# Optimization experiments

Hardware: AMD Instinct MI355X
Metric: run time of the kernel (lower is better)

Reference implementation:

```python
import jax, jax.numpy as jnp
import numpy as np

N, NODE_DIM, EDGE_DIM, HID, NREL = 1024, 128, 32, 128, 16


def _sage(h, adj, W, b):
    # agg = mean over (weighted) neighbors: (adj @ h) / (deg + 1e-6)
    agg = (adj @ h) / (jnp.sum(adj, axis=1, keepdims=True) + 1e-6)
    return jax.nn.relu(jnp.concatenate([h, agg], axis=1) @ W.T + b)


def setup_inputs() -> dict:
    key = jax.random.key(0)
    ks = jax.random.split(key, 12)
    s1 = 1.0 / np.sqrt(2 * NODE_DIM)
    s2 = 1.0 / np.sqrt(2 * HID)
    s3 = 1.0 / np.sqrt(2 * HID + EDGE_DIM)
    s4 = 1.0 / np.sqrt(HID)
    return {
        "node_feat": jax.random.normal(ks[0], (N, NODE_DIM), jnp.float32),
        "edge_feat": jax.random.normal(ks[1], (N, N, EDGE_DIM), jnp.float32),
        "adj": jax.random.uniform(ks[2], (N, N), jnp.float32),
        "W_g1": jax.random.normal(ks[3], (HID, 2 * NODE_DIM), jnp.float32) * s1,
        "b_g1": jax.random.normal(ks[4], (HID,), jnp.float32) * s1,
        "W_g2": jax.random.normal(ks[5], (HID, 2 * HID), jnp.float32) * s2,
        "b_g2": jax.random.normal(ks[6], (HID,), jnp.float32) * s2,
        "W_c1": jax.random.normal(ks[7], (HID, 2 * HID + EDGE_DIM), jnp.float32) * s3,
        "b_c1": jax.random.normal(ks[8], (HID,), jnp.float32) * s3,
        "W_c2": jax.random.normal(ks[9], (NREL, HID), jnp.float32) * s4,
        "b_c2": jax.random.normal(ks[10], (NREL,), jnp.float32) * s4,
    }


def reference(node_feat, edge_feat, adj, W_g1, b_g1, W_g2, b_g2, W_c1, b_c1, W_c2, b_c2):
    h = _sage(node_feat, adj, W_g1, b_g1)          # [N, HID]
    h = _sage(h, adj, W_g2, b_g2)                  # [N, HID]
    H = h.shape[1]
    # Split first classifier layer over [h_i ; h_j ; e_ij] to avoid a huge concat.
    Wa, Wb, We = W_c1[:, :H], W_c1[:, H:2 * H], W_c1[:, 2 * H:]
    pre = ((h @ Wa.T)[:, None, :]
           + (h @ Wb.T)[None, :, :]
           + jnp.einsum('ije,he->ijh', edge_feat, We)
           + b_c1)                                  # [N, N, HID]
    logits = jax.nn.relu(pre) @ W_c2.T + b_c2       # [N, N, NREL]
    # diagonal (i == j) stays zero, matching the skipped loop iterations
    n = logits.shape[0]
    mask = 1.0 - jnp.eye(n, dtype=logits.dtype)
    return logits * mask[:, :, None]
```

## Files before the change

### kernel.cpp

```cpp
#include <hip/hip_runtime.h>
#include <hip/hip_bf16.h>
#include <stdint.h>

constexpr int NN = 1024;
constexpr int DD = 128;
constexpr int EDIM = 32;
constexpr int NR = 16;

using short4v = __attribute__((ext_vector_type(4))) short;
using short8v = __attribute__((ext_vector_type(8))) short;
using f32x4   = __attribute__((ext_vector_type(4))) float;

__device__ __forceinline__ short f2bf(float x) {
  __hip_bfloat16 h = __float2bfloat16(x);
  return __builtin_bit_cast(short, h);
}

__device__ __forceinline__ void nt_store4(float* p, const float4& v) {
  f32x4 t;
  t[0] = v.x; t[1] = v.y; t[2] = v.z; t[3] = v.w;
  __builtin_nontemporal_store(t, (f32x4*)p);
}

__global__ __launch_bounds__(256) void k_adjmm(const float* __restrict__ X,
                                               const float* __restrict__ adj,
                                               float* __restrict__ part) {
  __shared__ short xt[32][264];
  int t = threadIdx.x;
  int w = t >> 6, lane = t & 63;
  int c = lane & 15, g = lane >> 4;
  int b = blockIdx.x;
  int ic = b & 15, hc = (b >> 4) & 3, kc = b >> 6;
  int i0 = ic * 64 + w * 16, h0 = hc * 32;
  int k0 = kc * 256;

  {
    const float* xr = X + (size_t)(k0 + t) * DD + h0;
    #pragma unroll
    for (int c8 = 0; c8 < 4; ++c8) {
      float4 v0 = *(const float4*)(xr + c8 * 8);
      float4 v1 = *(const float4*)(xr + c8 * 8 + 4);
      xt[c8 * 8 + 0][t] = f2bf(v0.x);
      xt[c8 * 8 + 1][t] = f2bf(v0.y);
      xt[c8 * 8 + 2][t] = f2bf(v0.z);
      xt[c8 * 8 + 3][t] = f2bf(v0.w);
      xt[c8 * 8 + 4][t] = f2bf(v1.x);
      xt[c8 * 8 + 5][t] = f2bf(v1.y);
      xt[c8 * 8 + 6][t] = f2bf(v1.z);
      xt[c8 * 8 + 7][t] = f2bf(v1.w);
    }
  }
  __syncthreads();

  f32x4 acc0 = {0, 0, 0, 0}, acc1 = {0, 0, 0, 0};
  const short* xa0 = &xt[c][8 * g];
  const short* xa1 = &xt[16 + c][8 * g];
  const float* ba  = adj + (size_t)(i0 + c) * NN + k0 + 8 * g;
  #pragma unroll
  for (int ks = 0; ks < 8; ++ks) {
    short8v a0 = *(const short8v*)(xa0 + ks * 32);
    short8v a1 = *(const short8v*)(xa1 + ks * 32);
    float4 b0 = *(const float4*)(ba + ks * 32);
    float4 b1 = *(const float4*)(ba + ks * 32 + 4);
    short8v bb;
    bb[0] = f2bf(b0.x); bb[1] = f2bf(b0.y); bb[2] = f2bf(b0.z); bb[3] = f2bf(b0.w);
    bb[4] = f2bf(b1.x); bb[5] = f2bf(b1.y); bb[6] = f2bf(b1.z); bb[7] = f2bf(b1.w);
    acc0 = __builtin_amdgcn_mfma_f32_16x16x32_bf16(a0, bb, acc0, 0, 0, 0);
    acc1 = __builtin_amdgcn_mfma_f32_16x16x32_bf16(a1, bb, acc1, 0, 0, 0);
  }
  float* p0 = part + ((size_t)kc * NN + (i0 + c)) * DD + h0 + 4 * g;
  float4 o0 = {acc0[0], acc0[1], acc0[2], acc0[3]};
  float4 o1 = {acc1[0], acc1[1], acc1[2], acc1[3]};
  *(float4*)(p0)      = o0;
  *(float4*)(p0 + 16) = o1;
}

__global__ __launch_bounds__(256) void k_dense1(const float* __restrict__ X,
                                                const float* __restrict__ part,
                                                const float* __restrict__ adj,
                                                const float* __restrict__ W,
                                                const float* __restrict__ b,
                                                float* __restrict__ out,
                                                float* __restrict__ rsinv) {
  __shared__ float sagg[2][128];
  __shared__ float red[4];
  int t = threadIdx.x;
  int ig = t >> 7, h = t & 127;
  int i = blockIdx.x * 2 + ig;
  {
    const float4* ar = (const float4*)(adj + (size_t)i * NN);
    float4 v0 = ar[h * 2], v1 = ar[h * 2 + 1];
    float s = v0.x + v0.y + v0.z + v0.w + v1.x + v1.y + v1.z + v1.w;
    #pragma unroll
    for (int off = 32; off > 0; off >>= 1) s += __shfl_down(s, off, 64);
    if ((t & 63) == 0) red[t >> 6] = s;
  }
  __syncthreads();
  float rs = 1.0f / (red[ig * 2] + red[ig * 2 + 1] + 1e-6f);
  if (h == 0) rsinv[i] = rs;
  {
    float ss = 0.f;
    #pragma unroll
    for (int kc = 0; kc < 4; ++kc) ss += part[(size_t)kc * NN * DD + (size_t)i * DD + h];
    sagg[ig][h] = ss * rs;
  }
  __syncthreads();
  const float4* xr = (const float4*)(X + (size_t)i * DD);
  const float4* ar = (const float4*)(&sagg[ig][0]);
  const float4* w1 = (const float4*)(W + (size_t)h * 256);
  const float4* w2 = (const float4*)(W + (size_t)h * 256 + DD);
  float acc = b[h];
  #pragma unroll 8
  for (int k = 0; k < 32; ++k) {
    float4 x = xr[k], w = w1[k];
    acc += x.x * w.x + x.y * w.y + x.z * w.z + x.w * w.w;
  }
  #pragma unroll 8
  for (int k = 0; k < 32; ++k) {
    float4 y = ar[k], w = w2[k];
    acc += y.x * w.x + y.y * w.y + y.z * w.z + y.w * w.w;
  }
  out[(size_t)i * DD + h] = fmaxf(acc, 0.f);
}

__global__ __launch_bounds__(256) void k_dense2ab(const float* __restrict__ X,
                                                  const float* __restrict__ part,
                                                  const float* __restrict__ rsinv,
                                                  const float* __restrict__ W,
                                                  const float* __restrict__ b,
                                                  const float* __restrict__ Wc1,
                                                  const float* __restrict__ bc1,
                                                  float* __restrict__ Aib,
                                                  float* __restrict__ Bmat) {
  __shared__ float sagg[2][128];
  __shared__ float sh2[2][128];
  int t = threadIdx.x;
  int ig = t >> 7, h = t & 127;
  int i = blockIdx.x * 2 + ig;
  {
    float ss = 0.f;
    #pragma unroll
    for (int kc = 0; kc < 4; ++kc) ss += part[(size_t)kc * NN * DD + (size_t)i * DD + h];
    sagg[ig][h] = ss * rsinv[i];
  }
  __syncthreads();
  {
    const float4* xr = (const float4*)(X + (size_t)i * DD);
    const float4* ar = (const float4*)(&sagg[ig][0]);
    const float4* w1 = (const float4*)(W + (size_t)h * 256);
    const float4* w2 = (const float4*)(W + (size_t)h * 256 + DD);
    float acc = b[h];
    #pragma unroll 8
    for (int k = 0; k < 32; ++k) {
      float4 x = xr[k], w = w1[k];
      acc += x.x * w.x + x.y * w.y + x.z * w.z + x.w * w.w;
    }
    #pragma unroll 8
    for (int k = 0; k < 32; ++k) {
      float4 y = ar[k], w = w2[k];
      acc += y.x * w.x + y.y * w.y + y.z * w.z + y.w * w.w;
    }
    sh2[ig][h] = fmaxf(acc, 0.f);
  }
  __syncthreads();
  const float4* xr = (const float4*)(&sh2[ig][0]);
  const float4* wa = (const float4*)(Wc1 + (size_t)h * 288);
  const float4* wb = (const float4*)(Wc1 + (size_t)h * 288 + 128);
  float aa = bc1[h], bb = 0.f;
  #pragma unroll 8
  for (int k = 0; k < 32; ++k) {
    float4 x = xr[k];
    float4 a = wa[k], b2 = wb[k];
    aa += x.x * a.x + x.y * a.y + x.z * a.z + x.w * a.w;
    bb += x.x * b2.x + x.y * b2.y + x.z * b2.z + x.w * b2.w;
  }
  Aib[(size_t)i * DD + h] = aa;
  Bmat[(size_t)i * DD + h] = bb;
}

#define EDGE_BODY(T, S, PF) do {                                              \
    float4 a_ = eA##S, b_ = eB##S;                                            \
    if (PF) {                                                                 \
      const float* p_ = ebl + (size_t)((T) + 6) * ((size_t)NN * EDIM);        \
      eA##S = *(const float4*)p_;                                             \
      eB##S = *(const float4*)(p_ + 4);                                       \
    }                                                                         \
    short8v ef_;                                                              \
    ef_[0]=f2bf(a_.x); ef_[1]=f2bf(a_.y); ef_[2]=f2bf(a_.z); ef_[3]=f2bf(a_.w); \
    ef_[4]=f2bf(b_.x); ef_[5]=f2bf(b_.y); ef_[6]=f2bf(b_.z); ef_[7]=f2bf(b_.w); \
    char* pw_ = psm + (((T) & 1) << 12);                                      \
    const float* ap_ = aibs + (T) * 128 + 4 * g;                              \
    _Pragma("unroll")                                                         \
    for (int n = 0; n < 8; ++n) {                                             \
      float4 av_ = *(const float4*)(ap_ + 16 * n);                            \
      f32x4 ci_;                                                              \
      ci_[0] = av_.x + bjv[n].x; ci_[1] = av_.y + bjv[n].y;                   \
      ci_[2] = av_.z + bjv[n].z; ci_[3] = av_.w + bjv[n].w;                   \
      f32x4 acc_ = __builtin_amdgcn_mfma_f32_16x16x32_bf16(weF[n], ef_, ci_, 0, 0, 0); \
      short4v pk_;                                                            \
      pk_[0] = f2bf(fmaxf(acc_[0], 0.f)); pk_[1] = f2bf(fmaxf(acc_[1], 0.f)); \
      pk_[2] = f2bf(fmaxf(acc_[2], 0.f)); pk_[3] = f2bf(fmaxf(acc_[3], 0.f)); \
      *(short4v*)(pw_ + (((n >> 1) << 10) + ((n & 1) << 9) + wroff)) = pk_;   \
    }                                                                         \
  } while (0)

#define G2(G2T, OREG) do {                                                    \
    f32x4 a2_;                                                                \
    a2_[0] = bc2v.x; a2_[1] = bc2v.y; a2_[2] = bc2v.z; a2_[3] = bc2v.w;       \
    const char* pp_ = psm + (((G2T) & 1) << 12);                              \
    _Pragma("unroll")                                                         \
    for (int kk = 0; kk < 4; ++kk) {                                          \
      short8v pb_ = *(const short8v*)(pp_ + ((kk << 10) + rdP));              \
      a2_ = __builtin_amdgcn_mfma_f32_16x16x32_bf16(wcF[kk], pb_, a2_, 0, 0, 0); \
    }                                                                         \
    bool dg_ = (j == i0 + (G2T));                                             \
    OREG.x = dg_ ? 0.f : a2_[0];                                              \
    OREG.y = dg_ ? 0.f : a2_[1];                                              \
    OREG.z = dg_ ? 0.f : a2_[2];                                              \
    OREG.w = dg_ ? 0.f : a2_[3];                                              \
  } while (0)

#define FLUSH(BASE) do {                                                      \
    nt_store4(out + ((size_t)(i0 + (BASE) + 0) * NN + j) * NR + 4 * g, o0);   \
    nt_store4(out + ((size_t)(i0 + (BASE) + 1) * NN + j) * NR + 4 * g, o1);   \
    nt_store4(out + ((size_t)(i0 + (BASE) + 2) * NN + j) * NR + 4 * g, o2);   \
    nt_store4(out + ((size_t)(i0 + (BASE) + 3) * NN + j) * NR + 4 * g, o3);   \
  } while (0)

__global__ __launch_bounds__(256, 1) void k_edge(const float* __restrict__ edge,
                                                 const float* __restrict__ Wc1,
                                                 const float* __restrict__ Wc2,
                                                 const float* __restrict__ bc2,
                                                 const float* __restrict__ Aib,
                                                 const float* __restrict__ Bmat,
                                                 float* __restrict__ out) {
  __shared__ __align__(16) char psm_all[4][2][4096];
  __shared__ __align__(16) float aibs[16 * 128];
  int tid = threadIdx.x;
  int w = tid >> 6, lane = tid & 63;
  int c = lane & 15, g = lane >> 4;
  int ig = blockIdx.x >> 4, jg = blockIdx.x & 15;
  int i0 = ig * 16;
  int j0w = jg * 64 + w * 16;
  int j = j0w + c;

  {
    int ii = tid >> 4, h8 = (tid & 15) * 8;
    const float4* s = (const float4*)(Aib + (size_t)(i0 + ii) * DD + h8);
    *(float4*)(aibs + ii * 128 + h8)     = s[0];
    *(float4*)(aibs + ii * 128 + h8 + 4) = s[1];
  }

  short8v weF[8];
  #pragma unroll
  for (int n = 0; n < 8; ++n) {
    const float* p = Wc1 + (size_t)(16 * n + c) * 288 + 256 + 8 * g;
    float4 f0 = *(const float4*)p;
    float4 f1 = *(const float4*)(p + 4);
    short8v s;
    s[0]=f2bf(f0.x); s[1]=f2bf(f0.y); s[2]=f2bf(f0.z); s[3]=f2bf(f0.w);
    s[4]=f2bf(f1.x); s[5]=f2bf(f1.y); s[6]=f2bf(f1.z); s[7]=f2bf(f1.w);
    weF[n] = s;
  }
  short8v wcF[4];
  #pragma unroll
  for (int kk = 0; kk < 4; ++kk) {
    const float* p = Wc2 + (size_t)c * DD + 32 * kk + 8 * g;
    float4 f0 = *(const float4*)p;
    float4 f1 = *(const float4*)(p + 4);
    short8v s;
    s[0]=f2bf(f0.x); s[1]=f2bf(f0.y); s[2]=f2bf(f0.z); s[3]=f2bf(f0.w);
    s[4]=f2bf(f1.x); s[5]=f2bf(f1.y); s[6]=f2bf(f1.z); s[7]=f2bf(f1.w);
    wcF[kk] = s;
  }
  float4 bc2v = *(const float4*)(bc2 + 4 * g);
  float4 bjv[8];
  #pragma unroll
  for (int n = 0; n < 8; ++n)
    bjv[n] = *(const float4*)(Bmat + (size_t)j * DD + 16 * n + 4 * g);

  __syncthreads();

  char* psm = &psm_all[w][0][0];
  const float* ebl = edge + ((size_t)i0 * NN + j) * EDIM + 8 * g;
  int wroff = (c << 4) + ((g & 1) << 3) + ((g >> 1) << 8);
  int rdP   = (g << 8) + (c << 4);

  float4 o0, o1, o2, o3;

  float4 eA0, eB0, eA1, eB1, eA2, eB2, eA3, eB3, eA4, eB4, eA5, eB5;
  {
    const size_t STP = (size_t)NN * EDIM;
    eA0 = *(const float4*)(ebl);            eB0 = *(const float4*)(ebl + 4);
    eA1 = *(const float4*)(ebl + STP);      eB1 = *(const float4*)(ebl + STP + 4);
    eA2 = *(const float4*)(ebl + 2 * STP);  eB2 = *(const float4*)(ebl + 2 * STP + 4);
    eA3 = *(const float4*)(ebl + 3 * STP);  eB3 = *(const float4*)(ebl + 3 * STP + 4);
    eA4 = *(const float4*)(ebl + 4 * STP);  eB4 = *(const float4*)(ebl + 4 * STP + 4);
    eA5 = *(const float4*)(ebl + 5 * STP);  eB5 = *(const float4*)(ebl + 5 * STP + 4);
  }

  EDGE_BODY(0, 0, 1);
  EDGE_BODY(1, 1, 1);  G2(0, o0);
  EDGE_BODY(2, 2, 1);  G2(1, o1);
  EDGE_BODY(3, 3, 1);  G2(2, o2);
  EDGE_BODY(4, 4, 1);  G2(3, o3);  FLUSH(0);
  EDGE_BODY(5, 5, 1);  G2(4, o0);
  EDGE_BODY(6, 0, 1);  G2(5, o1);
  EDGE_BODY(7, 1, 1);  G2(6, o2);
  EDGE_BODY(8, 2, 1);  G2(7, o3);  FLUSH(4);
  EDGE_BODY(9, 3, 1);  G2(8, o0);
  EDGE_BODY(10, 4, 0); G2(9, o1);
  EDGE_BODY(11, 5, 0); G2(10, o2);
  EDGE_BODY(12, 0, 0); G2(11, o3); FLUSH(8);
  EDGE_BODY(13, 1, 0); G2(12, o0);
  EDGE_BODY(14, 2, 0); G2(13, o1);
  EDGE_BODY(15, 3, 0); G2(14, o2);
  G2(15, o3); FLUSH(12);
}

extern "C" void kernel_launch(void* const* d_in, const int* in_sizes, int n_in,
                              void* d_out, int out_size, void* d_ws, size_t ws_size,
                              hipStream_t stream) {
  const float* node_feat = (const float*)d_in[0];
  const float* edge_feat = (const float*)d_in[1];
  const float* adj  = (const float*)d_in[2];
  const float* W_g1 = (const float*)d_in[3];
  const float* b_g1 = (const float*)d_in[4];
  const float* W_g2 = (const float*)d_in[5];
  const float* b_g2 = (const float*)d_in[6];
  const float* W_c1 = (const float*)d_in[7];
  const float* b_c1 = (const float*)d_in[8];
  const float* W_c2 = (const float*)d_in[9];
  const float* b_c2 = (const float*)d_in[10];
  float* out = (float*)d_out;

  float* ws    = (float*)d_ws;
  float* rsinv = ws;
  float* part  = ws + 1024;
  float* h1    = part + 4 * NN * DD;
  float* Aib   = h1 + NN * DD;
  float* Bmat  = Aib + NN * DD;

  k_adjmm<<<256, 256, 0, stream>>>(node_feat, adj, part);
  k_dense1<<<512, 256, 0, stream>>>(node_feat, part, adj, W_g1, b_g1, h1, rsinv);
  k_adjmm<<<256, 256, 0, stream>>>(h1, adj, part);
  k_dense2ab<<<512, 256, 0, stream>>>(h1, part, rsinv, W_g2, b_g2, W_c1, b_c1, Aib, Bmat);
  k_edge<<<1024, 256, 0, stream>>>(edge_feat, W_c1, W_c2, b_c2, Aib, Bmat, out);
}
```

Baseline: 115.4 us.

## Fuse four GNN prologue kernels into one cooperative kernel with grid syncs

Replaces the four separate launches (two adjacency matmuls and two dense layers) with a single cooperative kernel of 512 blocks that calls each stage body and separates the stages with grid-wide barriers. The aim is to remove per-launch overhead and inter-kernel gaps in the small prologue before the dominant edge kernel. In exchange it adds grid.sync costs, leaves half the blocks idle during the adjmm stages, and depends on all 512 blocks being co-resident.

```diff
diff --git a/kernel.cpp b/kernel.cpp
--- a/kernel.cpp
+++ b/kernel.cpp
@@ -1,6 +1,9 @@
 #include <hip/hip_runtime.h>
 #include <hip/hip_bf16.h>
+#include <hip/hip_cooperative_groups.h>
 #include <stdint.h>
+
+namespace cg = cooperative_groups;
 
 constexpr int NN = 1024;
 constexpr int DD = 128;
@@ -22,14 +25,14 @@
   __builtin_nontemporal_store(t, (f32x4*)p);
 }
 
-__global__ __launch_bounds__(256) void k_adjmm(const float* __restrict__ X,
-                                               const float* __restrict__ adj,
-                                               float* __restrict__ part) {
+
+__device__ void adjmm_body(int b, const float* __restrict__ X,
+                           const float* __restrict__ adj,
+                           float* __restrict__ part) {
   __shared__ short xt[32][264];
   int t = threadIdx.x;
   int w = t >> 6, lane = t & 63;
   int c = lane & 15, g = lane >> 4;
-  int b = blockIdx.x;
   int ic = b & 15, hc = (b >> 4) & 3, kc = b >> 6;
   int i0 = ic * 64 + w * 16, h0 = hc * 32;
   int k0 = kc * 256;
@@ -73,20 +76,21 @@
   float4 o1 = {acc1[0], acc1[1], acc1[2], acc1[3]};
   *(float4*)(p0)      = o0;
   *(float4*)(p0 + 16) = o1;
-}
-
-__global__ __launch_bounds__(256) void k_dense1(const float* __restrict__ X,
-                                                const float* __restrict__ part,
-                                                const float* __restrict__ adj,
-                                                const float* __restrict__ W,
-                                                const float* __restrict__ b,
-                                                float* __restrict__ out,
-                                                float* __restrict__ rsinv) {
+  __syncthreads();
+}
+
+__device__ void dense1_body(int b, const float* __restrict__ X,
+                            const float* __restrict__ part,
+                            const float* __restrict__ adj,
+                            const float* __restrict__ W,
+                            const float* __restrict__ bias,
+                            float* __restrict__ out,
+                            float* __restrict__ rsinv) {
   __shared__ float sagg[2][128];
   __shared__ float red[4];
   int t = threadIdx.x;
   int ig = t >> 7, h = t & 127;
-  int i = blockIdx.x * 2 + ig;
+  int i = b * 2 + ig;
   {
     const float4* ar = (const float4*)(adj + (size_t)i * NN);
     float4 v0 = ar[h * 2], v1 = ar[h * 2 + 1];
@@ -109,7 +113,7 @@
   const float4* ar = (const float4*)(&sagg[ig][0]);
   const float4* w1 = (const float4*)(W + (size_t)h * 256);
   const float4* w2 = (const float4*)(W + (size_t)h * 256 + DD);
-  float acc = b[h];
+  float acc = bias[h];
   #pragma unroll 8
   for (int k = 0; k < 32; ++k) {
     float4 x = xr[k], w = w1[k];
@@ -121,35 +125,36 @@
     acc += y.x * w.x + y.y * w.y + y.z * w.z + y.w * w.w;
   }
   out[(size_t)i * DD + h] = fmaxf(acc, 0.f);
-}
-
-__global__ __launch_bounds__(256) void k_dense2ab(const float* __restrict__ X,
-                                                  const float* __restrict__ part,
-                                                  const float* __restrict__ rsinv,
-                                                  const float* __restrict__ W,
-                                                  const float* __restrict__ b,
-                                                  const float* __restrict__ Wc1,
-                                                  const float* __restrict__ bc1,
-                                                  float* __restrict__ Aib,
-                                                  float* __restrict__ Bmat) {
-  __shared__ float sagg[2][128];
+  __syncthreads();
+}
+
+__device__ void dense2ab_body(int b, const float* __restrict__ X,
+                              const float* __restrict__ part,
+                              const float* __restrict__ rsinv,
+                              const float* __restrict__ W,
+                              const float* __restrict__ bias,
+                              const float* __restrict__ Wc1,
+                              const float* __restrict__ bc1,
+                              float* __restrict__ Aib,
+                              float* __restrict__ Bmat) {
+  __shared__ float sagg2[2][128];
   __shared__ float sh2[2][128];
   int t = threadIdx.x;
   int ig = t >> 7, h = t & 127;
-  int i = blockIdx.x * 2 + ig;
+  int i = b * 2 + ig;
   {
     float ss = 0.f;
     #pragma unroll
     for (int kc = 0; kc < 4; ++kc) ss += part[(size_t)kc * NN * DD + (size_t)i * DD + h];
-    sagg[ig][h] = ss * rsinv[i];
+    sagg2[ig][h] = ss * rsinv[i];
   }
   __syncthreads();
   {
     const float4* xr = (const float4*)(X + (size_t)i * DD);
-    const float4* ar = (const float4*)(&sagg[ig][0]);
+    const float4* ar = (const float4*)(&sagg2[ig][0]);
     const float4* w1 = (const float4*)(W + (size_t)h * 256);
     const float4* w2 = (const float4*)(W + (size_t)h * 256 + DD);
-    float acc = b[h];
+    float acc = bias[h];
     #pragma unroll 8
     for (int k = 0; k < 32; ++k) {
       float4 x = xr[k], w = w1[k];
@@ -176,6 +181,25 @@
   }
   Aib[(size_t)i * DD + h] = aa;
   Bmat[(size_t)i * DD + h] = bb;
+}
+
+__global__ __launch_bounds__(256, 2) void k_gnn(const float* node_feat,
+                                                const float* adj,
+                                                const float* W_g1, const float* b_g1,
+                                                const float* W_g2, const float* b_g2,
+                                                const float* W_c1, const float* b_c1,
+                                                float* part, float* h1,
+                                                float* Aib, float* Bmat,
+                                                float* rsinv) {
+  cg::grid_group grid = cg::this_grid();
+  int b = blockIdx.x;
+  if (b < 256) adjmm_body(b, node_feat, adj, part);
+  grid.sync();
+  dense1_body(b, node_feat, part, adj, W_g1, b_g1, h1, rsinv);
+  grid.sync();
+  if (b < 256) adjmm_body(b, h1, adj, part);
+  grid.sync();
+  dense2ab_body(b, h1, part, rsinv, W_g2, b_g2, W_c1, b_c1, Aib, Bmat);
 }
 
 #define EDGE_BODY(T, S, PF) do {                                              \
@@ -341,9 +365,13 @@
   float* Aib   = h1 + NN * DD;
   float* Bmat  = Aib + NN * DD;
 
-  k_adjmm<<<256, 256, 0, stream>>>(node_feat, adj, part);
-  k_dense1<<<512, 256, 0, stream>>>(node_feat, part, adj, W_g1, b_g1, h1, rsinv);
-  k_adjmm<<<256, 256, 0, stream>>>(h1, adj, part);
-  k_dense2ab<<<512, 256, 0, stream>>>(h1, part, rsinv, W_g2, b_g2, W_c1, b_c1, Aib, Bmat);
+  {
+    void* args[] = {(void*)&node_feat, (void*)&adj,
+                    (void*)&W_g1, (void*)&b_g1, (void*)&W_g2, (void*)&b_g2,
+                    (void*)&W_c1, (void*)&b_c1,
+                    (void*)&part, (void*)&h1, (void*)&Aib, (void*)&Bmat,
+                    (void*)&rsinv};
+    hipLaunchCooperativeKernel((void*)k_gnn, dim3(512), dim3(256), args, 0, stream);
+  }
   k_edge<<<1024, 256, 0, stream>>>(edge_feat, W_c1, W_c2, b_c2, Aib, Bmat, out);
 }
```

Measured after the change: 309.3 us. 168% more time.
